# Optimization experiments

Measured on AMD Instinct MI355X. Metric: run time of the kernel, lower is better.

Reference implementation:

```python
import jax, jax.numpy as jnp
import numpy as np

B, SQ, SV, D = 4, 4096, 4096, 64


def setup_inputs() -> dict:
    key = jax.random.key(0)
    kq, kv = jax.random.split(key)
    query = jax.random.normal(kq, (B, SQ, D), dtype=jnp.float32)
    value = jax.random.normal(kv, (B, SV, D), dtype=jnp.float32)
    return {"query": query, "value": value}


def reference(query, value):
    # scores: [B, Sq, Sv] = Q @ V^T  (no scale, no mask, as in the original)
    scores = jnp.einsum("bqd,bvd->bqv", query, value)
    weights = jax.nn.softmax(scores, axis=-1)
    # output: [B, Sq, D]
    return jnp.einsum("bqv,bvd->bqd", weights, value)
```

## Files before the change

kernel.cpp:

```cpp
#include <hip/hip_runtime.h>
#include <hip/hip_bf16.h>
#include <stdint.h>

#define BATCH 4
#define SQN   4096
#define SVN   4096
#define DIM   64
#define KT    32
#define NTILE (SVN / KT)
#define NSTEP 32

#define RMS 72
#define TRS 40
#define IMG_RM_H 0
#define IMG_RM_L 4608
#define IMG_TR_H 9216
#define IMG_TR_L 14336
#define BLOB     19456
#define NCHUNK   19
#define LDS_BYTES (8 * BLOB)

typedef __attribute__((ext_vector_type(8))) short bf16x8;
typedef __attribute__((ext_vector_type(4))) float f32x4;
typedef __attribute__((ext_vector_type(4))) unsigned int u32x4;

#if __has_builtin(__builtin_amdgcn_exp2f)
#define EXP2F __builtin_amdgcn_exp2f
#else
#define EXP2F exp2f
#endif

static __device__ __forceinline__ unsigned short bf16_rne(float x) {
  unsigned u = __float_as_uint(x);
  u += 0x7FFFu + ((u >> 16) & 1u);
  return (unsigned short)(u >> 16);
}
static __device__ __forceinline__ float bf16f(unsigned short h) {
  return __uint_as_float((unsigned)h << 16);
}
static __device__ __forceinline__ unsigned cvt_pk_bf16(float lo, float hi) {
  unsigned r;
  asm("v_cvt_pk_bf16_f32 %0, %1, %2" : "=v"(r) : "v"(lo), "v"(hi));
  return r;
}

__global__ __launch_bounds__(256) void vprep_kernel(const float* __restrict__ V,
                                                    char* __restrict__ ws) {
  __shared__ __align__(16) char sbuf[BLOB];
  const int b    = blockIdx.x >> 7;
  const int tile = blockIdx.x & 127;
  const int t    = threadIdx.x;
  const int vv   = t >> 3;
  const int d0   = (t & 7) * 8;

  const float* src = V + (((size_t)b * SVN + (size_t)tile * KT + vv) * DIM + d0);
  const float4 a0 = ((const float4*)src)[0];
  const float4 a1 = ((const float4*)src)[1];
  const float x[8] = {a0.x, a0.y, a0.z, a0.w, a1.x, a1.y, a1.z, a1.w};

  unsigned short h[8], l[8];
#pragma unroll
  for (int j = 0; j < 8; ++j) {
    h[j] = bf16_rne(x[j]);
    l[j] = bf16_rne(x[j] - bf16f(h[j]));
  }

  const int p = (((vv >> 2) & 1) << 4) | ((vv >> 3) << 2) | (vv & 3);
  bf16x8 vh, vl;
#pragma unroll
  for (int j = 0; j < 8; ++j) { vh[j] = (short)h[j]; vl[j] = (short)l[j]; }
  *(bf16x8*)(sbuf + IMG_RM_H + (p * RMS + d0) * 2) = vh;
  *(bf16x8*)(sbuf + IMG_RM_L + (p * RMS + d0) * 2) = vl;

  unsigned short* trh = (unsigned short*)(sbuf + IMG_TR_H);
  unsigned short* trl = (unsigned short*)(sbuf + IMG_TR_L);
#pragma unroll
  for (int j = 0; j < 8; ++j) {
    trh[(d0 + j) * TRS + vv] = h[j];
    trl[(d0 + j) * TRS + vv] = l[j];
  }
  __syncthreads();

  float4* dst = (float4*)(ws + (size_t)(b * NTILE + tile) * BLOB);
  const float4* s4 = (const float4*)sbuf;
#pragma unroll
  for (int k = 0; k < 5; ++k) {
    const int idx = t + k * 256;
    if (idx < BLOB / 16) dst[idx] = s4[idx];
  }
}

__global__ __launch_bounds__(512, 2) void attn_kernel(const float* __restrict__ Qg,
                                                      const char* __restrict__ vprep,
                                                      float* __restrict__ out) {
  extern __shared__ char smem[];
  const int raw = blockIdx.x;
  const int lb = (raw & 7) * 32 + (raw >> 3);
  const int batch = lb >> 6;
  const int qbase = (lb & 63) * 64;
  const int tid = threadIdx.x;
  const int lane = tid & 63;
  const int wid = tid >> 6;
  const int qt = wid & 1;
  const int quarter = wid >> 1;
  const int lr = lane & 15;
  const int lg = lane >> 4;

  bf16x8 Qh[2][2], Ql[2][2];
#pragma unroll
  for (int qb = 0; qb < 2; ++qb) {
    const size_t qrow = (size_t)batch * SQN + qbase + qt * 32 + qb * 16 + lr;
#pragma unroll
    for (int ks = 0; ks < 2; ++ks) {
      const float* qp = Qg + qrow * DIM + ks * 32 + 8 * lg;
      const float4 f0 = ((const float4*)qp)[0];
      const float4 f1 = ((const float4*)qp)[1];
      const float xv[8] = {f0.x, f0.y, f0.z, f0.w, f1.x, f1.y, f1.z, f1.w};
#pragma unroll
      for (int j = 0; j < 8; ++j) {
        const float v = xv[j] * 1.44269504088896f;
        const unsigned short hh = bf16_rne(v);
        Qh[qb][ks][j] = (short)hh;
        Ql[qb][ks][j] = (short)bf16_rne(v - bf16f(hh));
      }
    }
  }

  f32x4 Oacc[2][4];
#pragma unroll
  for (int qb = 0; qb < 2; ++qb)
#pragma unroll
    for (int db = 0; db < 4; ++db) Oacc[qb][db] = (f32x4){0.f, 0.f, 0.f, 0.f};
  float m_[2] = {-1e30f, -1e30f};
  float l_[2] = {0.f, 0.f};

  const size_t tb0 = (size_t)(batch * NTILE) * BLOB;
  const int sq = wid >> 1;
  const int sh = wid & 1;

  auto stage = [&](int t, int b) {
#pragma unroll
    for (int k = 0; k < 10; ++k) {
      const int sub = sh + 2 * k;
      if (sub < NCHUNK) {
        const char* g = vprep + tb0 + (size_t)(sq * NSTEP + t) * BLOB + sub * 1024 + lane * 16;
        char* lp = smem + (sq * 2 + b) * BLOB + sub * 1024;
        __builtin_amdgcn_global_load_lds(
            (const __attribute__((address_space(1))) unsigned int*)g,
            (__attribute__((address_space(3))) unsigned int*)lp, 16, 0, 0);
      }
    }
  };

  stage(0, 0);
  __syncthreads();
  int buf = 0;

  for (int t = 0; t < NSTEP; ++t) {
    if (t + 1 < NSTEP) stage(t + 1, buf ^ 1);

    const char* qbuf = smem + (quarter * 2 + buf) * BLOB;

    bf16x8 Vh[2][2], Vl[2][2];
#pragma unroll
    for (int vt = 0; vt < 2; ++vt)
#pragma unroll
      for (int ks = 0; ks < 2; ++ks) {
        const int off = ((vt * 16 + lr) * RMS + ks * 32 + 8 * lg) * 2;
        Vh[vt][ks] = *(const bf16x8*)(qbuf + IMG_RM_H + off);
        Vl[vt][ks] = *(const bf16x8*)(qbuf + IMG_RM_L + off);
      }

    f32x4 sacc[2][2];
#pragma unroll
    for (int qb = 0; qb < 2; ++qb)
#pragma unroll
      for (int vt = 0; vt < 2; ++vt) {
        f32x4 acc = (f32x4){0.f, 0.f, 0.f, 0.f};
#pragma unroll
        for (int ks = 0; ks < 2; ++ks) {
          acc = __builtin_amdgcn_mfma_f32_16x16x32_bf16(Vh[vt][ks], Qh[qb][ks], acc, 0, 0, 0);
          acc = __builtin_amdgcn_mfma_f32_16x16x32_bf16(Vh[vt][ks], Ql[qb][ks], acc, 0, 0, 0);
          acc = __builtin_amdgcn_mfma_f32_16x16x32_bf16(Vl[vt][ks], Qh[qb][ks], acc, 0, 0, 0);
        }
        sacc[qb][vt] = acc;
      }

    bf16x8 Ph[2], Pl[2];
#pragma unroll
    for (int qb = 0; qb < 2; ++qb) {
      float mt = -1e30f;
#pragma unroll
      for (int vt = 0; vt < 2; ++vt)
#pragma unroll
        for (int r = 0; r < 4; ++r) mt = fmaxf(mt, sacc[qb][vt][r]);
      mt = fmaxf(mt, __shfl_xor(mt, 16, 64));
      mt = fmaxf(mt, __shfl_xor(mt, 32, 64));
      const float mnew = fmaxf(m_[qb], mt);
      const float alpha = EXP2F(m_[qb] - mnew);
      float p[8];
      float rs = 0.f;
#pragma unroll
      for (int vt = 0; vt < 2; ++vt)
#pragma unroll
        for (int r = 0; r < 4; ++r) {
          const float pv = EXP2F(sacc[qb][vt][r] - mnew);
          p[vt * 4 + r] = pv;
          rs += pv;
        }
      rs += __shfl_xor(rs, 16, 64);
      rs += __shfl_xor(rs, 32, 64);
      l_[qb] = l_[qb] * alpha + rs;
      m_[qb] = mnew;
#pragma unroll
      for (int db = 0; db < 4; ++db) Oacc[qb][db] *= alpha;
      u32x4 hu, lu;
#pragma unroll
      for (int j = 0; j < 4; ++j) {
        const unsigned hd = cvt_pk_bf16(p[2 * j], p[2 * j + 1]);
        const float h0 = __uint_as_float(hd << 16);
        const float h1 = __uint_as_float(hd & 0xFFFF0000u);
        hu[j] = hd;
        lu[j] = cvt_pk_bf16(p[2 * j] - h0, p[2 * j + 1] - h1);
      }
      Ph[qb] = __builtin_bit_cast(bf16x8, hu);
      Pl[qb] = __builtin_bit_cast(bf16x8, lu);
    }

#pragma unroll
    for (int db = 0; db < 4; ++db) {
      const int toff = ((db * 16 + lr) * TRS + 8 * lg) * 2;
      const bf16x8 Ah = *(const bf16x8*)(qbuf + IMG_TR_H + toff);
      const bf16x8 Al = *(const bf16x8*)(qbuf + IMG_TR_L + toff);
#pragma unroll
      for (int qb = 0; qb < 2; ++qb) {
        Oacc[qb][db] = __builtin_amdgcn_mfma_f32_16x16x32_bf16(Ah, Ph[qb], Oacc[qb][db], 0, 0, 0);
        Oacc[qb][db] = __builtin_amdgcn_mfma_f32_16x16x32_bf16(Al, Ph[qb], Oacc[qb][db], 0, 0, 0);
        Oacc[qb][db] = __builtin_amdgcn_mfma_f32_16x16x32_bf16(Ah, Pl[qb], Oacc[qb][db], 0, 0, 0);
      }
    }

    __syncthreads();
    buf ^= 1;
  }

  float* mbuf = (float*)smem;
  float* mlb  = (float*)(smem + 2 * 4 * 32 * 68 * 4);
#pragma unroll
  for (int qb = 0; qb < 2; ++qb) {
    const int q = qb * 16 + lr;
    float* dst = mbuf + ((qt * 4 + quarter) * 32 + q) * 68;
#pragma unroll
    for (int db = 0; db < 4; ++db)
#pragma unroll
      for (int r = 0; r < 4; ++r) dst[db * 16 + 4 * lg + r] = Oacc[qb][db][r];
  }
  if (lg == 0) {
#pragma unroll
    for (int qb = 0; qb < 2; ++qb) {
      const int q = qb * 16 + lr;
      mlb[((qt * 4 + quarter) * 32 + q) * 2 + 0] = m_[qb];
      mlb[((qt * 4 + quarter) * 32 + q) * 2 + 1] = l_[qb];
    }
  }
  __syncthreads();

  const int q_all = tid >> 3;
  const int d0 = (tid & 7) * 8;
  const int qt2 = q_all >> 5;
  const int qq = q_all & 31;
  float M = -1e30f;
#pragma unroll
  for (int w = 0; w < 4; ++w) M = fmaxf(M, mlb[((qt2 * 4 + w) * 32 + qq) * 2]);
  float L = 0.f;
  float o[8] = {0, 0, 0, 0, 0, 0, 0, 0};
#pragma unroll
  for (int w = 0; w < 4; ++w) {
    const float a = EXP2F(mlb[((qt2 * 4 + w) * 32 + qq) * 2] - M);
    L += a * mlb[((qt2 * 4 + w) * 32 + qq) * 2 + 1];
    const float* srcp = mbuf + ((qt2 * 4 + w) * 32 + qq) * 68 + d0;
#pragma unroll
    for (int j = 0; j < 8; ++j) o[j] += a * srcp[j];
  }
  const float inv = 1.0f / L;
  float* op = out + ((size_t)batch * SQN + qbase + qt2 * 32 + qq) * DIM + d0;
  float4 w0 = {o[0] * inv, o[1] * inv, o[2] * inv, o[3] * inv};
  float4 w1 = {o[4] * inv, o[5] * inv, o[6] * inv, o[7] * inv};
  ((float4*)op)[0] = w0;
  ((float4*)op)[1] = w1;
}

extern "C" void kernel_launch(void* const* d_in, const int* in_sizes, int n_in,
                              void* d_out, int out_size, void* d_ws, size_t ws_size,
                              hipStream_t stream) {
  const float* Qg = (const float*)d_in[0];
  const float* Vg = (const float*)d_in[1];
  float* out = (float*)d_out;
  char* ws = (char*)d_ws;
  const size_t need = (size_t)BATCH * NTILE * BLOB;
  if (ws_size < need) return;

  hipFuncSetAttribute((const void*)attn_kernel,
                      hipFuncAttributeMaxDynamicSharedMemorySize, LDS_BYTES);

  vprep_kernel<<<BATCH * NTILE, 256, 0, stream>>>(Vg, ws);
  attn_kernel<<<256, 512, LDS_BYTES, stream>>>(Qg, ws, out);
}
```

Measured before the change: 134.4 us.

## Split V staging into row-major and transposed halves with fine-grained waits

The V prep kernel now writes the row-major and transposed bf16 images straight to global memory, using a lane shuffle to pack pairs, instead of going through LDS. The attention loop stages the row-major and transposed chunks as separate groups and waits on vmcnt counts with raw barriers. This lets the QK^T step start before the transposed image has landed. It also adds s_setprio around the MFMA blocks and a lazy softmax rescale that skips the rescale unless the max grows by more than 8. The hand-set vmcnt values and the lazy-rescale threshold add correctness risk.

```diff
diff --git a/kernel.cpp b/kernel.cpp
--- a/kernel.cpp
+++ b/kernel.cpp
@@ -17,7 +17,6 @@
 #define IMG_TR_H 9216
 #define IMG_TR_L 14336
 #define BLOB     19456
-#define NCHUNK   19
 #define LDS_BYTES (8 * BLOB)
 
 typedef __attribute__((ext_vector_type(8))) short bf16x8;
@@ -46,7 +45,6 @@
 
 __global__ __launch_bounds__(256) void vprep_kernel(const float* __restrict__ V,
                                                     char* __restrict__ ws) {
-  __shared__ __align__(16) char sbuf[BLOB];
   const int b    = blockIdx.x >> 7;
   const int tile = blockIdx.x & 127;
   const int t    = threadIdx.x;
@@ -65,28 +63,27 @@
     l[j] = bf16_rne(x[j] - bf16f(h[j]));
   }
 
+  char* blob = ws + (size_t)(b * NTILE + tile) * BLOB;
+
   const int p = (((vv >> 2) & 1) << 4) | ((vv >> 3) << 2) | (vv & 3);
   bf16x8 vh, vl;
 #pragma unroll
   for (int j = 0; j < 8; ++j) { vh[j] = (short)h[j]; vl[j] = (short)l[j]; }
-  *(bf16x8*)(sbuf + IMG_RM_H + (p * RMS + d0) * 2) = vh;
-  *(bf16x8*)(sbuf + IMG_RM_L + (p * RMS + d0) * 2) = vl;
-
-  unsigned short* trh = (unsigned short*)(sbuf + IMG_TR_H);
-  unsigned short* trl = (unsigned short*)(sbuf + IMG_TR_L);
+  *(bf16x8*)(blob + IMG_RM_H + (p * RMS + d0) * 2) = vh;
+  *(bf16x8*)(blob + IMG_RM_L + (p * RMS + d0) * 2) = vl;
+
+  const bool even = (vv & 1) == 0;
 #pragma unroll
   for (int j = 0; j < 8; ++j) {
-    trh[(d0 + j) * TRS + vv] = h[j];
-    trl[(d0 + j) * TRS + vv] = l[j];
-  }
-  __syncthreads();
-
-  float4* dst = (float4*)(ws + (size_t)(b * NTILE + tile) * BLOB);
-  const float4* s4 = (const float4*)sbuf;
-#pragma unroll
-  for (int k = 0; k < 5; ++k) {
-    const int idx = t + k * 256;
-    if (idx < BLOB / 16) dst[idx] = s4[idx];
+    const unsigned own = ((unsigned)l[j] << 16) | (unsigned)h[j];
+    const unsigned got = (unsigned)__shfl_xor((int)own, 8, 64);
+    if (even) {
+      const unsigned d = (unsigned)h[j] | ((got & 0xFFFFu) << 16);
+      *(unsigned*)(blob + IMG_TR_H + ((d0 + j) * TRS + vv) * 2) = d;
+    } else {
+      const unsigned d = (got >> 16) | (own & 0xFFFF0000u);
+      *(unsigned*)(blob + IMG_TR_L + ((d0 + j) * TRS + (vv - 1)) * 2) = d;
+    }
   }
 }
 
@@ -138,26 +135,42 @@
   const int sq = wid >> 1;
   const int sh = wid & 1;
 
-  auto stage = [&](int t, int b) {
-#pragma unroll
-    for (int k = 0; k < 10; ++k) {
-      const int sub = sh + 2 * k;
-      if (sub < NCHUNK) {
-        const char* g = vprep + tb0 + (size_t)(sq * NSTEP + t) * BLOB + sub * 1024 + lane * 16;
-        char* lp = smem + (sq * 2 + b) * BLOB + sub * 1024;
-        __builtin_amdgcn_global_load_lds(
-            (const __attribute__((address_space(1))) unsigned int*)g,
-            (__attribute__((address_space(3))) unsigned int*)lp, 16, 0, 0);
-      }
+  auto stage_rm = [&](int t, int b) {
+    const size_t g0 = tb0 + (size_t)(sq * NSTEP + t) * BLOB;
+    char* l0 = smem + (sq * 2 + b) * BLOB;
+    const int c0 = sh * 4;
+#pragma unroll
+    for (int k = 0; k < 5; ++k) {
+      const int sub = c0 + k;
+      __builtin_amdgcn_global_load_lds(
+          (const __attribute__((address_space(1))) unsigned int*)(vprep + g0 + sub * 1024 + lane * 16),
+          (__attribute__((address_space(3))) unsigned int*)(l0 + sub * 1024), 16, 0, 0);
     }
   };
-
-  stage(0, 0);
-  __syncthreads();
+  auto stage_tr = [&](int t, int b) {
+    const size_t g0 = tb0 + (size_t)(sq * NSTEP + t) * BLOB;
+    char* l0 = smem + (sq * 2 + b) * BLOB;
+    const int c0 = 9 + sh * 5;
+#pragma unroll
+    for (int k = 0; k < 5; ++k) {
+      const int sub = c0 + k;
+      __builtin_amdgcn_global_load_lds(
+          (const __attribute__((address_space(1))) unsigned int*)(vprep + g0 + sub * 1024 + lane * 16),
+          (__attribute__((address_space(3))) unsigned int*)(l0 + sub * 1024), 16, 0, 0);
+    }
+  };
+
+  stage_rm(0, 0);
+  stage_tr(0, 0);
   int buf = 0;
 
   for (int t = 0; t < NSTEP; ++t) {
-    if (t + 1 < NSTEP) stage(t + 1, buf ^ 1);
+    asm volatile("s_waitcnt vmcnt(5)" ::: "memory");
+    __builtin_amdgcn_s_barrier();
+    if (t + 1 < NSTEP) {
+      stage_rm(t + 1, buf ^ 1);
+      stage_tr(t + 1, buf ^ 1);
+    }
 
     const char* qbuf = smem + (quarter * 2 + buf) * BLOB;
 
@@ -172,6 +185,7 @@
       }
 
     f32x4 sacc[2][2];
+    __builtin_amdgcn_s_setprio(1);
 #pragma unroll
     for (int qb = 0; qb < 2; ++qb)
 #pragma unroll
@@ -185,6 +199,7 @@
         }
         sacc[qb][vt] = acc;
       }
+    __builtin_amdgcn_s_setprio(0);
 
     bf16x8 Ph[2], Pl[2];
 #pragma unroll
@@ -196,24 +211,40 @@
         for (int r = 0; r < 4; ++r) mt = fmaxf(mt, sacc[qb][vt][r]);
       mt = fmaxf(mt, __shfl_xor(mt, 16, 64));
       mt = fmaxf(mt, __shfl_xor(mt, 32, 64));
-      const float mnew = fmaxf(m_[qb], mt);
-      const float alpha = EXP2F(m_[qb] - mnew);
+
       float p[8];
       float rs = 0.f;
-#pragma unroll
-      for (int vt = 0; vt < 2; ++vt)
-#pragma unroll
-        for (int r = 0; r < 4; ++r) {
-          const float pv = EXP2F(sacc[qb][vt][r] - mnew);
-          p[vt * 4 + r] = pv;
-          rs += pv;
-        }
-      rs += __shfl_xor(rs, 16, 64);
-      rs += __shfl_xor(rs, 32, 64);
-      l_[qb] = l_[qb] * alpha + rs;
-      m_[qb] = mnew;
-#pragma unroll
-      for (int db = 0; db < 4; ++db) Oacc[qb][db] *= alpha;
+      if (__any(mt > m_[qb] + 8.0f)) {
+        const float mnew = fmaxf(m_[qb], mt);
+        const float alpha = EXP2F(m_[qb] - mnew);
+#pragma unroll
+        for (int vt = 0; vt < 2; ++vt)
+#pragma unroll
+          for (int r = 0; r < 4; ++r) {
+            const float pv = EXP2F(sacc[qb][vt][r] - mnew);
+            p[vt * 4 + r] = pv;
+            rs += pv;
+          }
+        rs += __shfl_xor(rs, 16, 64);
+        rs += __shfl_xor(rs, 32, 64);
+        l_[qb] = l_[qb] * alpha + rs;
+        m_[qb] = mnew;
+#pragma unroll
+        for (int db = 0; db < 4; ++db) Oacc[qb][db] *= alpha;
+      } else {
+#pragma unroll
+        for (int vt = 0; vt < 2; ++vt)
+#pragma unroll
+          for (int r = 0; r < 4; ++r) {
+            const float pv = EXP2F(sacc[qb][vt][r] - m_[qb]);
+            p[vt * 4 + r] = pv;
+            rs += pv;
+          }
+        rs += __shfl_xor(rs, 16, 64);
+        rs += __shfl_xor(rs, 32, 64);
+        l_[qb] += rs;
+      }
+
       u32x4 hu, lu;
 #pragma unroll
       for (int j = 0; j < 4; ++j) {
@@ -227,6 +258,13 @@
       Pl[qb] = __builtin_bit_cast(bf16x8, lu);
     }
 
+    if (t + 1 < NSTEP)
+      asm volatile("s_waitcnt vmcnt(10)" ::: "memory");
+    else
+      asm volatile("s_waitcnt vmcnt(0)" ::: "memory");
+    __builtin_amdgcn_s_barrier();
+
+    __builtin_amdgcn_s_setprio(1);
 #pragma unroll
     for (int db = 0; db < 4; ++db) {
       const int toff = ((db * 16 + lr) * TRS + 8 * lg) * 2;
@@ -239,10 +277,12 @@
         Oacc[qb][db] = __builtin_amdgcn_mfma_f32_16x16x32_bf16(Ah, Pl[qb], Oacc[qb][db], 0, 0, 0);
       }
     }
-
-    __syncthreads();
+    __builtin_amdgcn_s_setprio(0);
+
     buf ^= 1;
   }
+
+  __syncthreads();
 
   float* mbuf = (float*)smem;
   float* mlb  = (float*)(smem + 2 * 4 * 32 * 68 * 4);
```

Result: slower. 138.1 us (+2.7%).
